# Performance work log

Hardware: AMD Instinct MI355X
Metric: run time of the kernel (lower is better)

Reference implementation:

```python
import jax, jax.numpy as jnp
import numpy as np
import math

B, N, K, S = 4, 128, 250, 250   # batch, channels(d_model), chunk len, num chunks
M = 64 // 2                      # d_state complex modes (conjugate-pair S4D param.)


def setup_inputs() -> dict:
    key = jax.random.key(0)
    ks = jax.random.split(key, 24)
    d = {"x": jax.random.normal(ks[0], (B, N, K, S), jnp.float32)}
    i = 1
    for p in ("intra", "inter"):
        # S4D (diagonal SSM) parameters
        d[p + "_log_dt"] = (jax.random.uniform(ks[i], (N,), jnp.float32)
                            * (math.log(0.1) - math.log(0.001)) + math.log(0.001))
        d[p + "_logA_re"] = jnp.full((N, M), math.log(0.5), jnp.float32)
        d[p + "_A_im"] = jnp.tile(math.pi * jnp.arange(M, dtype=jnp.float32), (N, 1))
        d[p + "_C_re"] = jax.random.normal(ks[i + 1], (N, M), jnp.float32) * (0.5 ** 0.5)
        d[p + "_C_im"] = jax.random.normal(ks[i + 2], (N, M), jnp.float32) * (0.5 ** 0.5)
        d[p + "_D"] = jax.random.normal(ks[i + 3], (N,), jnp.float32)
        # S4 output position-wise linear (H -> 2H) + GLU
        d[p + "_ow"] = jax.random.normal(ks[i + 4], (2 * N, N), jnp.float32) / math.sqrt(N)
        d[p + "_ob"] = jnp.zeros((2 * N,), jnp.float32)
        # block linear
        d[p + "_lw"] = jax.random.normal(ks[i + 5], (N, N), jnp.float32) / math.sqrt(N)
        d[p + "_lb"] = jnp.zeros((N,), jnp.float32)
        # GroupNorm(1, N)
        d[p + "_gg"] = jnp.ones((N,), jnp.float32)
        d[p + "_gb"] = jnp.zeros((N,), jnp.float32)
        i += 6
    return d


def _s4(u, log_dt, logA_re, A_im, C_re, C_im, D, ow, ob):
    # u: [b, H, L] (transposed layout). S4D kernel + FFT conv + GELU + GLU out.
    L = u.shape[-1]
    dt = jnp.exp(log_dt)                              # [H]
    A = -jnp.exp(logA_re) + 1j * A_im                 # [H, M]
    dtA = dt[:, None] * A                             # [H, M]
    C = (C_re + 1j * C_im) * (jnp.exp(dtA) - 1.0) / A # ZOH-discretized C
    vand = jnp.exp(dtA[:, :, None] * jnp.arange(L, dtype=jnp.float32))  # [H, M, L]
    kern = 2.0 * jnp.einsum('hm,hml->hl', C, vand).real                 # [H, L]
    n = 2 * L
    y = jnp.fft.irfft(jnp.fft.rfft(u, n) * jnp.fft.rfft(kern, n), n)[..., :L]
    y = y + D[:, None] * u
    y = jax.nn.gelu(y)
    y = jnp.einsum('oh,bhl->bol', ow, y) + ob[None, :, None]            # [b, 2H, L]
    y1, y2 = jnp.split(y, 2, axis=1)
    return y1 * jax.nn.sigmoid(y2)                                      # GLU -> [b, H, L]


def _group_norm(x, g, b, eps=1e-8):
    mu = jnp.mean(x, axis=(1, 2, 3), keepdims=True)
    var = jnp.var(x, axis=(1, 2, 3), keepdims=True)
    return (x - mu) / jnp.sqrt(var + eps) * g[None, :, None, None] + b[None, :, None, None]


def reference(x,
              intra_log_dt, intra_logA_re, intra_A_im, intra_C_re, intra_C_im,
              intra_D, intra_ow, intra_ob, intra_lw, intra_lb, intra_gg, intra_gb,
              inter_log_dt, inter_logA_re, inter_A_im, inter_C_re, inter_C_im,
              inter_D, inter_ow, inter_ob, inter_lw, inter_lb, inter_gg, inter_gb):
    Bx, Nx, Kx, Sx = x.shape
    # intra (within-chunk) path: sequence length = K
    intra = jnp.transpose(x, (0, 3, 1, 2)).reshape(Bx * Sx, Nx, Kx)
    intra = _s4(intra, intra_log_dt, intra_logA_re, intra_A_im,
                intra_C_re, intra_C_im, intra_D, intra_ow, intra_ob)
    # faithful to torch: .view(B*S*K, -1) on contiguous [B*S, N, K]
    intra = (intra.reshape(Bx * Sx * Kx, -1) @ intra_lw.T + intra_lb).reshape(Bx * Sx, Nx, Kx)
    intra = jnp.transpose(intra.reshape(Bx, Sx, Nx, Kx), (0, 2, 3, 1))  # [B,N,K,S]
    intra = _group_norm(intra, intra_gg, intra_gb) + x
    # inter (across-chunk) path: sequence length = S
    inter = jnp.transpose(intra, (0, 2, 1, 3)).reshape(Bx * Kx, Nx, Sx)
    inter = _s4(inter, inter_log_dt, inter_logA_re, inter_A_im,
                inter_C_re, inter_C_im, inter_D, inter_ow, inter_ob)
    inter = (inter.reshape(Bx * Kx * Sx, -1) @ inter_lw.T + inter_lb).reshape(Bx * Kx, Nx, Sx)
    inter = jnp.transpose(inter.reshape(Bx, Kx, Nx, Sx), (0, 2, 1, 3))  # [B,N,K,S]
    inter = _group_norm(inter, inter_gg, inter_gb)
    return inter + intra
```

## Files before the change

kernel.cpp:

```cpp
#include <hip/hip_runtime.h>
#include <math.h>

#define NTOT 32000000

typedef __attribute__((ext_vector_type(8))) short bf8_t;
typedef __attribute__((ext_vector_type(4))) float f4_t;

__device__ __forceinline__ float fast_tanh(float t) {
    return 1.0f - 2.0f / (1.0f + __expf(2.0f * t));
}
__device__ __forceinline__ float gelu_f(float v) {
    return 0.5f * v * (1.0f + fast_tanh(0.7978845608028654f * (v + 0.044715f * v * v * v)));
}
__device__ __forceinline__ float sigmoid_f(float v) {
    return 1.0f / (1.0f + __expf(-v));
}
__device__ __forceinline__ unsigned short f2bf(float f) {
    unsigned u = __float_as_uint(f);
    u = (u + 0x7FFFu + ((u >> 16) & 1u)) >> 16;
    return (unsigned short)u;
}
__device__ __forceinline__ float bf2f(unsigned short u) {
    return __uint_as_float(((unsigned)u) << 16);
}
__device__ __forceinline__ unsigned swz(unsigned a) {
    return a ^ (((a >> 9) & 7u) << 4);
}

__global__ void wc_kernel(const float* __restrict__ log_dt, const float* __restrict__ logA_re,
                          const float* __restrict__ A_im, const float* __restrict__ C_re,
                          const float* __restrict__ C_im, float* __restrict__ wC) {
    int t = blockIdx.x * 256 + threadIdx.x;
    if (t >= 128 * 32) return;
    int h = t >> 5, m = t & 31;
    float dt  = expf(log_dt[h]);
    float are = -expf(logA_re[t]);
    float aim = A_im[t];
    float er  = expf(dt * are);
    float wr  = er * cosf(dt * aim);
    float wi  = er * sinf(dt * aim);
    float e1r = wr - 1.0f, e1i = wi;
    float inv = 1.0f / (are * are + aim * aim);
    float qr  = (e1r * are + e1i * aim) * inv;
    float qi  = (e1i * are - e1r * aim) * inv;
    float cre = C_re[t], cim = C_im[t];
    wC[h * 128 + m]      = dt * are;
    wC[h * 128 + 32 + m] = dt * aim;
    wC[h * 128 + 64 + m] = 2.0f * (cre * qr - cim * qi);
    wC[h * 128 + 96 + m] = 2.0f * (cre * qi + cim * qr);
}

__global__ void kern_kernel(const float* __restrict__ wC, float* __restrict__ kern) {
    int h = blockIdx.x, l = threadIdx.x;
    const float* wc = wC + (h << 7);
    float acc = 0.0f;
    if (l < 250) {
        float fl = (float)l;
#pragma unroll 1
        for (int m = 0; m < 32; ++m) {
            float er  = expf(wc[m] * fl);
            float ang = wc[32 + m] * fl;
            float sv, cv;
            sincosf(ang, &sv, &cv);
            acc += er * (wc[64 + m] * cv - wc[96 + m] * sv);
        }
    }
    kern[(h << 8) + l] = acc;
}

__global__ void cvtw_kernel(const float* __restrict__ ow, const float* __restrict__ lw,
                            unsigned short* __restrict__ owbf, unsigned short* __restrict__ lwbf) {
    int t = blockIdx.x * 256 + threadIdx.x;
    if (t < 32768) owbf[t] = f2bf(ow[t]);
    else if (t < 49152) lwbf[t - 32768] = f2bf(lw[t - 32768]);
}

__global__ __launch_bounds__(256, 2)
void conv_kernel(const float* __restrict__ in, unsigned short* __restrict__ Y,
                 const float* __restrict__ kern, const float* __restrict__ Dv, int inter) {
    __shared__ unsigned short Bhi[128 * 264];
    __shared__ unsigned short Blo[128 * 40];
    __shared__ float klds[512];
    const int tid = threadIdx.x;
    const int lane = tid & 63, wave = tid >> 6;
    const int lid = lane & 15, quad = lane >> 4;
    const int s0 = blockIdx.x * 128;
    const int h = blockIdx.y, b = blockIdx.z;
    klds[tid] = 0.0f;
    klds[256 + tid] = kern[(h << 8) + tid];
    const float Dh = Dv[h];
    const float* src = in + (long)(b * 128 + h) * 62500;

    f4_t acc[4][8];
#pragma unroll
    for (int rt = 0; rt < 4; ++rt)
#pragma unroll
        for (int ct = 0; ct < 8; ++ct) acc[rt][ct] = (f4_t)0.0f;

    float2 pf[8];
    auto loadc = [&](int c) {
        if (!inter) {
#pragma unroll
            for (int it = 0; it < 8; ++it) {
                int kk = (tid >> 6) + (it << 2);
                int k = (c << 5) + kk;
                int ss = (tid & 63) << 1;
                bool v = (k < 250) && (s0 + ss < 250);
                pf[it] = v ? *(const float2*)(src + (long)k * 250 + s0 + ss)
                           : make_float2(0.0f, 0.0f);
            }
        } else {
#pragma unroll
            for (int it = 0; it < 8; ++it) {
                int kk2 = (tid >> 4) + (it << 4);
                int cc = (tid & 15) << 1;
                bool v = (s0 + kk2 < 250) && ((c << 5) + cc < 250);
                pf[it] = v ? *(const float2*)(src + (long)(s0 + kk2) * 250 + (c << 5) + cc)
                           : make_float2(0.0f, 0.0f);
            }
        }
    };
    auto storec = [&](int c) {
        if (!inter) {
#pragma unroll
            for (int it = 0; it < 8; ++it) {
                int kk = (tid >> 6) + (it << 2);
                int k = (c << 5) + kk;
                int ss = (tid & 63) << 1;
                unsigned short hx = f2bf(pf[it].x);
                unsigned short hy = f2bf(pf[it].y);
                Bhi[ss * 264 + k] = hx;
                Bhi[(ss + 1) * 264 + k] = hy;
                Blo[ss * 40 + kk] = f2bf(pf[it].x - bf2f(hx));
                Blo[(ss + 1) * 40 + kk] = f2bf(pf[it].y - bf2f(hy));
            }
        } else {
#pragma unroll
            for (int it = 0; it < 8; ++it) {
                int kk2 = (tid >> 4) + (it << 4);
                int cc = (tid & 15) << 1;
                int k = (c << 5) + cc;
                unsigned short hx = f2bf(pf[it].x);
                unsigned short hy = f2bf(pf[it].y);
                Bhi[kk2 * 264 + k] = hx;
                Bhi[kk2 * 264 + k + 1] = hy;
                Blo[kk2 * 40 + cc] = f2bf(pf[it].x - bf2f(hx));
                Blo[kk2 * 40 + cc + 1] = f2bf(pf[it].y - bf2f(hy));
            }
        }
    };

    loadc(0);
#pragma unroll 1
    for (int c = 0; c < 8; ++c) {
        __syncthreads();
        storec(c);
        __syncthreads();
        if (c < 7) loadc(c + 1);
        const int c32 = c << 5;
        bf8_t ah[4], al[4];
#pragma unroll
        for (int rt = 0; rt < 4; ++rt) {
            const int R = (rt << 6) + (wave << 4);
            if (c32 <= R + 15) {
                int d0 = 256 + R + lid - c32 - (quad << 3) - 7;
                float r[8];
#pragma unroll
                for (int j = 0; j < 8; ++j) r[j] = klds[d0 + j];
#pragma unroll
                for (int j = 0; j < 8; ++j) {
                    float v = r[7 - j];
                    unsigned short hb = f2bf(v);
                    ah[rt][j] = (short)hb;
                    al[rt][j] = (short)f2bf(v - bf2f(hb));
                }
            }
        }
#pragma unroll
        for (int ct = 0; ct < 8; ++ct) {
            bf8_t bh = *(const bf8_t*)(Bhi + (ct * 16 + lid) * 264 + c32 + (quad << 3));
            bf8_t bl = *(const bf8_t*)(Blo + (ct * 16 + lid) * 40 + (quad << 3));
#pragma unroll
            for (int rt = 0; rt < 4; ++rt) {
                const int R = (rt << 6) + (wave << 4);
                if (c32 <= R + 15) {
                    acc[rt][ct] = __builtin_amdgcn_mfma_f32_16x16x32_bf16(ah[rt], bh, acc[rt][ct], 0, 0, 0);
                    acc[rt][ct] = __builtin_amdgcn_mfma_f32_16x16x32_bf16(ah[rt], bl, acc[rt][ct], 0, 0, 0);
                    acc[rt][ct] = __builtin_amdgcn_mfma_f32_16x16x32_bf16(al[rt], bh, acc[rt][ct], 0, 0, 0);
                }
            }
        }
    }
    __syncthreads();
#pragma unroll
    for (int rt = 0; rt < 4; ++rt) {
        const int Rq = (rt << 6) + (wave << 4) + (quad << 2);
#pragma unroll
        for (int ct = 0; ct < 8; ++ct) {
            const int sl = ct * 16 + lid;
#pragma unroll
            for (int reg = 0; reg < 4; ++reg) {
                int row = Rq + reg;
                float u = bf2f(Bhi[sl * 264 + row]);
                float y = acc[rt][ct][reg] + Dh * u;
                Bhi[sl * 264 + row] = f2bf(gelu_f(y));
            }
        }
    }
    __syncthreads();
    const unsigned int* Bu = (const unsigned int*)Bhi;
    unsigned int* Yg = (unsigned int*)Y + ((long)(b * 250 + s0) * 128 + h) * 125;
#pragma unroll 1
    for (int i = tid; i < 16384; i += 256) {
        int sl = i >> 7, e = i & 127;
        if (e < 125 && s0 + sl < 250)
            Yg[(long)sl * 16000 + e] = Bu[sl * 132 + e];
    }
}

__global__ __launch_bounds__(256, 2)
void mlp_kernel(const unsigned short* __restrict__ Ybf, const unsigned short* __restrict__ owbf,
                const float* __restrict__ ob, const unsigned short* __restrict__ lwbf,
                const float* __restrict__ lb, float* __restrict__ V, double* __restrict__ part) {
    __shared__ unsigned short ZL[32768];
    __shared__ unsigned short Yt[32 * 136];
    const int tid = threadIdx.x;
    const int lane = tid & 63, wave = tid >> 6;
    const int lid = lane & 15, quad = lane >> 4;
    const int seq = blockIdx.x;
    const unsigned short* Ys = Ybf + (long)seq * 32000;

    const int tb0 = 2 * wave;
    int tmap[4] = {tb0, tb0 + 1, tb0 + 8, tb0 + 9};
    bf8_t wf[4][4];
#pragma unroll
    for (int c = 0; c < 4; ++c)
#pragma unroll
        for (int t = 0; t < 4; ++t)
            wf[c][t] = *(const bf8_t*)(owbf + (tmap[t] * 16 + lid) * 128 + c * 32 + quad * 8);
    float ob1[2][4], ob2[2][4];
#pragma unroll
    for (int p = 0; p < 2; ++p)
#pragma unroll
        for (int reg = 0; reg < 4; ++reg) {
            int o = tmap[p] * 16 + quad * 4 + reg;
            ob1[p][reg] = ob[o];
            ob2[p][reg] = ob[128 + o];
        }

    unsigned int pf[8];
    auto loadc = [&](int l0) {
#pragma unroll
        for (int it = 0; it < 8; ++it) {
            int i = tid + it * 256;
            int h = i >> 4;
            int l = l0 + (i & 15) * 2;
            pf[it] = (l < 250) ? *(const unsigned int*)(Ys + h * 250 + l) : 0u;
        }
    };
    auto storec = [&]() {
#pragma unroll
        for (int it = 0; it < 8; ++it) {
            int i = tid + it * 256;
            int h = i >> 4;
            int l2 = (i & 15) * 2;
            Yt[l2 * 136 + h] = (unsigned short)(pf[it] & 0xFFFF);
            Yt[(l2 + 1) * 136 + h] = (unsigned short)(pf[it] >> 16);
        }
    };

    loadc(0);
#pragma unroll 1
    for (int ch = 0; ch < 8; ++ch) {
        __syncthreads();
        storec();
        __syncthreads();
        if (ch < 7) loadc((ch + 1) * 32);
        f4_t acc[4][2];
#pragma unroll
        for (int t = 0; t < 4; ++t)
#pragma unroll
            for (int jj = 0; jj < 2; ++jj) acc[t][jj] = (f4_t)0.0f;
#pragma unroll
        for (int c = 0; c < 4; ++c) {
            bf8_t bfr[2];
#pragma unroll
            for (int jj = 0; jj < 2; ++jj)
                bfr[jj] = *(const bf8_t*)(Yt + (jj * 16 + lid) * 136 + c * 32 + quad * 8);
#pragma unroll
            for (int t = 0; t < 4; ++t)
#pragma unroll
                for (int jj = 0; jj < 2; ++jj)
                    acc[t][jj] = __builtin_amdgcn_mfma_f32_16x16x32_bf16(wf[c][t], bfr[jj], acc[t][jj], 0, 0, 0);
        }
        const int lbase = ch * 32;
#pragma unroll
        for (int p = 0; p < 2; ++p) {
            int ob0 = tmap[p] * 16 + quad * 4;
#pragma unroll
            for (int reg = 0; reg < 4; ++reg) {
                int o = ob0 + reg;
#pragma unroll
                for (int jj = 0; jj < 2; ++jj) {
                    int l = lbase + jj * 16 + lid;
                    if (l < 250) {
                        float z1 = acc[p][jj][reg] + ob1[p][reg];
                        float z2 = acc[p + 2][jj][reg] + ob2[p][reg];
                        unsigned a = swz((unsigned)(o * 250 + l) * 2u);
                        *(unsigned short*)((char*)ZL + a) = f2bf(z1 * sigmoid_f(z2));
                    }
                }
            }
        }
    }
    __syncthreads();

    f4_t acc2[4][8];
#pragma unroll
    for (int mt = 0; mt < 4; ++mt)
#pragma unroll
        for (int nt = 0; nt < 8; ++nt) acc2[mt][nt] = (f4_t)0.0f;
    const int j0 = wave * 64;
#pragma unroll
    for (int c = 0; c < 4; ++c) {
        bf8_t af[4];
#pragma unroll
        for (int mt = 0; mt < 4; ++mt) {
            unsigned a = swz((unsigned)((j0 + mt * 16 + lid) * 128 + c * 32 + quad * 8) * 2u);
            af[mt] = *(const bf8_t*)((char*)ZL + a);
        }
#pragma unroll
        for (int nt = 0; nt < 8; ++nt) {
            bf8_t bfr = *(const bf8_t*)(lwbf + (nt * 16 + lid) * 128 + c * 32 + quad * 8);
#pragma unroll
            for (int mt = 0; mt < 4; ++mt)
                acc2[mt][nt] = __builtin_amdgcn_mfma_f32_16x16x32_bf16(af[mt], bfr, acc2[mt][nt], 0, 0, 0);
        }
    }
    double s = 0.0, q = 0.0;
    float* Vs = V + (long)seq * 32000;
#pragma unroll
    for (int nt = 0; nt < 8; ++nt) {
        int o = nt * 16 + lid;
        float bb = lb[o];
#pragma unroll
        for (int mt = 0; mt < 4; ++mt)
#pragma unroll
            for (int reg = 0; reg < 4; ++reg) {
                int j = j0 + mt * 16 + quad * 4 + reg;
                if (j < 250) {
                    float v = acc2[mt][nt][reg] + bb;
                    Vs[j * 128 + o] = v;
                    s += (double)v;
                    q += (double)v * (double)v;
                }
            }
    }
    __syncthreads();
    double* red = (double*)Yt;
    red[tid] = s;
    red[256 + tid] = q;
    __syncthreads();
    for (int st = 128; st > 0; st >>= 1) {
        if (tid < st) {
            red[tid] += red[tid + st];
            red[256 + tid] += red[256 + tid + st];
        }
        __syncthreads();
    }
    if (tid == 0) {
        part[seq * 2] = red[0];
        part[seq * 2 + 1] = red[256];
    }
}

__global__ void stats_final_kernel(const double* __restrict__ part, float* __restrict__ stats) {
    __shared__ double ssum[256], ssq[256];
    const int b = blockIdx.x;
    double s = 0.0, q = 0.0;
    if (threadIdx.x < 250) {
        s = part[(b * 250 + threadIdx.x) * 2];
        q = part[(b * 250 + threadIdx.x) * 2 + 1];
    }
    ssum[threadIdx.x] = s; ssq[threadIdx.x] = q;
    __syncthreads();
    for (int st = 128; st > 0; st >>= 1) {
        if (threadIdx.x < st) {
            ssum[threadIdx.x] += ssum[threadIdx.x + st];
            ssq[threadIdx.x]  += ssq[threadIdx.x + st];
        }
        __syncthreads();
    }
    if (threadIdx.x == 0) {
        double mu = ssum[0] / 8000000.0;
        double var = ssq[0] / 8000000.0 - mu * mu;
        stats[b * 2] = (float)mu;
        stats[b * 2 + 1] = (float)(1.0 / sqrt(var + 1e-8));
    }
}

__global__ void intra_fin_kernel(const float* __restrict__ f, const float* __restrict__ x,
                                 const float* __restrict__ stats, const float* __restrict__ gg,
                                 const float* __restrict__ gb, float* __restrict__ out) {
    __shared__ float tile[32][33];
    int kt = blockIdx.x, st = blockIdx.y;
    int bn = blockIdx.z; int b = bn >> 7, n = bn & 127;
    int tx = threadIdx.x & 31, ty = threadIdx.x >> 5;
    const float mu = stats[b * 2], rs = stats[b * 2 + 1];
    const float ga = gg[n] * rs, bb = gb[n];
    const float* fb = f + (long)(b * 250) * 32000 + n * 250;
#pragma unroll
    for (int j = 0; j < 4; ++j) {
        int k = kt * 32 + tx;
        int s = st * 32 + ty + j * 8;
        if (k < 250 && s < 250) tile[ty + j * 8][tx] = fb[(long)s * 32000 + k];
    }
    __syncthreads();
#pragma unroll
    for (int j = 0; j < 4; ++j) {
        int s = st * 32 + tx;
        int k = kt * 32 + ty + j * 8;
        if (k < 250 && s < 250) {
            long idx = ((long)(b * 128 + n) * 250 + k) * 250 + s;
            out[idx] = (tile[tx][ty + j * 8] - mu) * ga + bb + x[idx];
        }
    }
}

__global__ void final_kernel(const float* __restrict__ f2, const float* __restrict__ stats,
                             const float* __restrict__ gg, const float* __restrict__ gb,
                             float* __restrict__ out) {
    long g = (long)blockIdx.x * 256 + threadIdx.x;
    if (g >= NTOT) return;
    int s = (int)(g % 250); long r = g / 250;
    int k = (int)(r % 250); long bn = r / 250;
    int n = (int)(bn % 128); int b = (int)(bn / 128);
    float mu = stats[b * 2], rs = stats[b * 2 + 1];
    float v = f2[((long)(b * 250 + k) * 128 + n) * 250 + s];
    out[g] = (v - mu) * rs * gg[n] + gb[n] + out[g];
}

extern "C" void kernel_launch(void* const* d_in, const int* in_sizes, int n_in,
                              void* d_out, int out_size, void* d_ws, size_t ws_size,
                              hipStream_t stream) {
    (void)in_sizes; (void)n_in; (void)out_size; (void)ws_size;
    const float* x = (const float*)d_in[0];
    float* out = (float*)d_out;
    char* base = (char*)d_ws;
    float* V            = (float*)base;
    unsigned short* Ybf = (unsigned short*)(base + 128000000L);
    float* wC           = (float*)(base + 256000000L);
    unsigned short* owbf= (unsigned short*)(base + 256065536L);
    unsigned short* lwbf= (unsigned short*)(base + 256131072L);
    double* part        = (double*)(base + 256163840L);
    float* stats        = (float*)(base + 256180224L);
    float* kern         = (float*)(base + 120000000L);

    const float* i_logdt = (const float*)d_in[1];
    const float* i_logA  = (const float*)d_in[2];
    const float* i_Aim   = (const float*)d_in[3];
    const float* i_Cre   = (const float*)d_in[4];
    const float* i_Cim   = (const float*)d_in[5];
    const float* i_D     = (const float*)d_in[6];
    const float* i_ow    = (const float*)d_in[7];
    const float* i_ob    = (const float*)d_in[8];
    const float* i_lw    = (const float*)d_in[9];
    const float* i_lb    = (const float*)d_in[10];
    const float* i_gg    = (const float*)d_in[11];
    const float* i_gb    = (const float*)d_in[12];
    const float* e_logdt = (const float*)d_in[13];
    const float* e_logA  = (const float*)d_in[14];
    const float* e_Aim   = (const float*)d_in[15];
    const float* e_Cre   = (const float*)d_in[16];
    const float* e_Cim   = (const float*)d_in[17];
    const float* e_D     = (const float*)d_in[18];
    const float* e_ow    = (const float*)d_in[19];
    const float* e_ob    = (const float*)d_in[20];
    const float* e_lw    = (const float*)d_in[21];
    const float* e_lb    = (const float*)d_in[22];
    const float* e_gg    = (const float*)d_in[23];
    const float* e_gb    = (const float*)d_in[24];

    wc_kernel<<<16, 256, 0, stream>>>(i_logdt, i_logA, i_Aim, i_Cre, i_Cim, wC);
    kern_kernel<<<128, 256, 0, stream>>>(wC, kern);
    cvtw_kernel<<<192, 256, 0, stream>>>(i_ow, i_lw, owbf, lwbf);
    conv_kernel<<<dim3(2, 128, 4), 256, 0, stream>>>(x, Ybf, kern, i_D, 0);
    mlp_kernel<<<1000, 256, 0, stream>>>(Ybf, owbf, i_ob, lwbf, i_lb, V, part);
    stats_final_kernel<<<4, 256, 0, stream>>>(part, stats);
    intra_fin_kernel<<<dim3(8, 8, 512), 256, 0, stream>>>(V, x, stats, i_gg, i_gb, out);

    wc_kernel<<<16, 256, 0, stream>>>(e_logdt, e_logA, e_Aim, e_Cre, e_Cim, wC);
    kern_kernel<<<128, 256, 0, stream>>>(wC, kern);
    cvtw_kernel<<<192, 256, 0, stream>>>(e_ow, e_lw, owbf, lwbf);
    conv_kernel<<<dim3(2, 128, 4), 256, 0, stream>>>(out, Ybf, kern, e_D, 1);
    mlp_kernel<<<1000, 256, 0, stream>>>(Ybf, owbf, e_ob, lwbf, e_lb, V, part);
    stats_final_kernel<<<4, 256, 0, stream>>>(part, stats);
    final_kernel<<<NTOT / 256, 256, 0, stream>>>(V, stats, e_gg, e_gb, out);
}
```

Baseline: 811.4 us.

## Precompute Toeplitz kernel fragments and retile causal conv with swizzled LDS

Folds the D skip term into kernel tap zero and adds a frag_kernel that precomputes hi/lo bf16 MFMA A-fragments of the Toeplitz convolution matrix in global memory. The conv kernel then loads those fragments directly instead of rebuilding them per block from LDS. The conv tile shrinks to 64 sequences per block with a new wave-to-tile mapping, doubling the grid and allowing 3 blocks per CU. The input tile moves to an XOR-swizzled unpadded LDS layout with packed stores, and the epilogue no longer re-reads u for the D term. The cost is an extra small launch and global fragment reads, which are likely to hit in L2.

```diff
diff --git a/kernel.cpp b/kernel.cpp
--- a/kernel.cpp
+++ b/kernel.cpp
@@ -50,7 +50,8 @@
     wC[h * 128 + 96 + m] = 2.0f * (cre * qi + cim * qr);
 }
 
-__global__ void kern_kernel(const float* __restrict__ wC, float* __restrict__ kern) {
+__global__ void kern_kernel(const float* __restrict__ wC, const float* __restrict__ Dv,
+                            float* __restrict__ kern) {
     int h = blockIdx.x, l = threadIdx.x;
     const float* wc = wC + (h << 7);
     float acc = 0.0f;
@@ -64,8 +65,28 @@
             sincosf(ang, &sv, &cv);
             acc += er * (wc[64 + m] * cv - wc[96 + m] * sv);
         }
+        if (l == 0) acc += Dv[h];
     }
     kern[(h << 8) + l] = acc;
+}
+
+__global__ void frag_kernel(const float* __restrict__ kern, unsigned short* __restrict__ fragH,
+                            unsigned short* __restrict__ fragL) {
+    int h = blockIdx.x, d16 = blockIdx.y, lane = threadIdx.x;
+    int lid = lane & 15, q = lane >> 4;
+    const float* kh = kern + (h << 8);
+    bf8_t vh, vl;
+#pragma unroll
+    for (int j = 0; j < 8; ++j) {
+        int idx = d16 * 16 + lid - 8 * q - j;
+        float v = (idx >= 0) ? kh[idx] : 0.0f;
+        unsigned short hb = f2bf(v);
+        vh[j] = (short)hb;
+        vl[j] = (short)f2bf(v - bf2f(hb));
+    }
+    long off = ((long)((h << 4) + d16) * 64 + lane) * 8;
+    *(bf8_t*)(fragH + off) = vh;
+    *(bf8_t*)(fragL + off) = vl;
 }
 
 __global__ void cvtw_kernel(const float* __restrict__ ow, const float* __restrict__ lw,
@@ -75,47 +96,50 @@
     else if (t < 49152) lwbf[t - 32768] = f2bf(lw[t - 32768]);
 }
 
-__global__ __launch_bounds__(256, 2)
+__global__ __launch_bounds__(256, 3)
 void conv_kernel(const float* __restrict__ in, unsigned short* __restrict__ Y,
-                 const float* __restrict__ kern, const float* __restrict__ Dv, int inter) {
-    __shared__ unsigned short Bhi[128 * 264];
-    __shared__ unsigned short Blo[128 * 40];
-    __shared__ float klds[512];
+                 const unsigned short* __restrict__ fragH, const unsigned short* __restrict__ fragL,
+                 int inter) {
+    __shared__ unsigned short Bhi[64 * 256];
+    __shared__ unsigned short Blo[64 * 40];
     const int tid = threadIdx.x;
     const int lane = tid & 63, wave = tid >> 6;
     const int lid = lane & 15, quad = lane >> 4;
-    const int s0 = blockIdx.x * 128;
+    const int a = wave >> 1, p = wave & 1;
+    const int s0 = blockIdx.x * 64;
     const int h = blockIdx.y, b = blockIdx.z;
-    klds[tid] = 0.0f;
-    klds[256 + tid] = kern[(h << 8) + tid];
-    const float Dh = Dv[h];
     const float* src = in + (long)(b * 128 + h) * 62500;
-
-    f4_t acc[4][8];
+    char* BhiB = (char*)Bhi;
+    char* BloB = (char*)Blo;
+
+    f4_t acc[4][4];
 #pragma unroll
     for (int rt = 0; rt < 4; ++rt)
 #pragma unroll
-        for (int ct = 0; ct < 8; ++ct) acc[rt][ct] = (f4_t)0.0f;
-
-    float2 pf[8];
+        for (int ct = 0; ct < 4; ++ct) acc[rt][ct] = (f4_t)0.0f;
+
+    float2 pf[4];
     auto loadc = [&](int c) {
         if (!inter) {
 #pragma unroll
-            for (int it = 0; it < 8; ++it) {
-                int kk = (tid >> 6) + (it << 2);
+            for (int it = 0; it < 4; ++it) {
+                int i = tid + it * 256;
+                int kk = i >> 5;
+                int sp = (i & 31) << 1;
                 int k = (c << 5) + kk;
-                int ss = (tid & 63) << 1;
-                bool v = (k < 250) && (s0 + ss < 250);
-                pf[it] = v ? *(const float2*)(src + (long)k * 250 + s0 + ss)
+                bool v = (k < 250) && (s0 + sp < 250);
+                pf[it] = v ? *(const float2*)(src + (long)k * 250 + s0 + sp)
                            : make_float2(0.0f, 0.0f);
             }
         } else {
 #pragma unroll
-            for (int it = 0; it < 8; ++it) {
-                int kk2 = (tid >> 4) + (it << 4);
-                int cc = (tid & 15) << 1;
-                bool v = (s0 + kk2 < 250) && ((c << 5) + cc < 250);
-                pf[it] = v ? *(const float2*)(src + (long)(s0 + kk2) * 250 + (c << 5) + cc)
+            for (int it = 0; it < 4; ++it) {
+                int i = tid + it * 256;
+                int sq = i >> 4;
+                int tt = (i & 15) << 1;
+                int t = (c << 5) + tt;
+                bool v = (s0 + sq < 250) && (t < 250);
+                pf[it] = v ? *(const float2*)(src + (long)(s0 + sq) * 250 + t)
                            : make_float2(0.0f, 0.0f);
             }
         }
@@ -123,29 +147,34 @@
     auto storec = [&](int c) {
         if (!inter) {
 #pragma unroll
-            for (int it = 0; it < 8; ++it) {
-                int kk = (tid >> 6) + (it << 2);
+            for (int it = 0; it < 4; ++it) {
+                int i = tid + it * 256;
+                int kk = i >> 5;
+                int sp = (i & 31) << 1;
                 int k = (c << 5) + kk;
-                int ss = (tid & 63) << 1;
                 unsigned short hx = f2bf(pf[it].x);
                 unsigned short hy = f2bf(pf[it].y);
-                Bhi[ss * 264 + k] = hx;
-                Bhi[(ss + 1) * 264 + k] = hy;
-                Blo[ss * 40 + kk] = f2bf(pf[it].x - bf2f(hx));
-                Blo[(ss + 1) * 40 + kk] = f2bf(pf[it].y - bf2f(hy));
+                unsigned b0 = (unsigned)(sp * 512 + k * 2) ^ ((unsigned)(sp & 7) << 4);
+                unsigned b1 = (unsigned)((sp + 1) * 512 + k * 2) ^ ((unsigned)((sp + 1) & 7) << 4);
+                *(unsigned short*)(BhiB + b0) = hx;
+                *(unsigned short*)(BhiB + b1) = hy;
+                Blo[sp * 40 + kk] = f2bf(pf[it].x - bf2f(hx));
+                Blo[(sp + 1) * 40 + kk] = f2bf(pf[it].y - bf2f(hy));
             }
         } else {
 #pragma unroll
-            for (int it = 0; it < 8; ++it) {
-                int kk2 = (tid >> 4) + (it << 4);
-                int cc = (tid & 15) << 1;
-                int k = (c << 5) + cc;
+            for (int it = 0; it < 4; ++it) {
+                int i = tid + it * 256;
+                int sq = i >> 4;
+                int tt = (i & 15) << 1;
                 unsigned short hx = f2bf(pf[it].x);
                 unsigned short hy = f2bf(pf[it].y);
-                Bhi[kk2 * 264 + k] = hx;
-                Bhi[kk2 * 264 + k + 1] = hy;
-                Blo[kk2 * 40 + cc] = f2bf(pf[it].x - bf2f(hx));
-                Blo[kk2 * 40 + cc + 1] = f2bf(pf[it].y - bf2f(hy));
+                unsigned hpack = (unsigned)hx | ((unsigned)hy << 16);
+                unsigned b0 = (unsigned)(sq * 512 + ((c << 5) + tt) * 2) ^ ((unsigned)(sq & 7) << 4);
+                *(unsigned*)(BhiB + b0) = hpack;
+                unsigned short lx = f2bf(pf[it].x - bf2f(hx));
+                unsigned short ly = f2bf(pf[it].y - bf2f(hy));
+                *(unsigned*)(BloB + sq * 80 + tt * 2) = (unsigned)lx | ((unsigned)ly << 16);
             }
         }
     };
@@ -157,64 +186,54 @@
         storec(c);
         __syncthreads();
         if (c < 7) loadc(c + 1);
-        const int c32 = c << 5;
-        bf8_t ah[4], al[4];
+        bf8_t bh[4], bl[4];
+#pragma unroll
+        for (int ct = 0; ct < 4; ++ct) {
+            int row = ct * 16 + lid;
+            unsigned byteB = (unsigned)(row * 512 + c * 64 + quad * 16) ^ ((unsigned)(row & 7) << 4);
+            bh[ct] = *(const bf8_t*)(BhiB + byteB);
+            bl[ct] = *(const bf8_t*)(BloB + row * 80 + quad * 16);
+        }
 #pragma unroll
         for (int rt = 0; rt < 4; ++rt) {
-            const int R = (rt << 6) + (wave << 4);
-            if (c32 <= R + 15) {
-                int d0 = 256 + R + lid - c32 - (quad << 3) - 7;
-                float r[8];
-#pragma unroll
-                for (int j = 0; j < 8; ++j) r[j] = klds[d0 + j];
-#pragma unroll
-                for (int j = 0; j < 8; ++j) {
-                    float v = r[7 - j];
-                    unsigned short hb = f2bf(v);
-                    ah[rt][j] = (short)hb;
-                    al[rt][j] = (short)f2bf(v - bf2f(hb));
+            int n = 2 * rt + a - c;
+            if (n >= 0) {
+                long fo = ((long)((h << 4) + 2 * n + p) * 64 + lane) * 8;
+                bf8_t fh = *(const bf8_t*)(fragH + fo);
+                bf8_t fl = *(const bf8_t*)(fragL + fo);
+#pragma unroll
+                for (int ct = 0; ct < 4; ++ct) {
+                    acc[rt][ct] = __builtin_amdgcn_mfma_f32_16x16x32_bf16(fh, bh[ct], acc[rt][ct], 0, 0, 0);
+                    acc[rt][ct] = __builtin_amdgcn_mfma_f32_16x16x32_bf16(fh, bl[ct], acc[rt][ct], 0, 0, 0);
+                    acc[rt][ct] = __builtin_amdgcn_mfma_f32_16x16x32_bf16(fl, bh[ct], acc[rt][ct], 0, 0, 0);
                 }
             }
         }
-#pragma unroll
-        for (int ct = 0; ct < 8; ++ct) {
-            bf8_t bh = *(const bf8_t*)(Bhi + (ct * 16 + lid) * 264 + c32 + (quad << 3));
-            bf8_t bl = *(const bf8_t*)(Blo + (ct * 16 + lid) * 40 + (quad << 3));
-#pragma unroll
-            for (int rt = 0; rt < 4; ++rt) {
-                const int R = (rt << 6) + (wave << 4);
-                if (c32 <= R + 15) {
-                    acc[rt][ct] = __builtin_amdgcn_mfma_f32_16x16x32_bf16(ah[rt], bh, acc[rt][ct], 0, 0, 0);
-                    acc[rt][ct] = __builtin_amdgcn_mfma_f32_16x16x32_bf16(ah[rt], bl, acc[rt][ct], 0, 0, 0);
-                    acc[rt][ct] = __builtin_amdgcn_mfma_f32_16x16x32_bf16(al[rt], bh, acc[rt][ct], 0, 0, 0);
-                }
-            }
-        }
     }
     __syncthreads();
 #pragma unroll
     for (int rt = 0; rt < 4; ++rt) {
-        const int Rq = (rt << 6) + (wave << 4) + (quad << 2);
-#pragma unroll
-        for (int ct = 0; ct < 8; ++ct) {
-            const int sl = ct * 16 + lid;
-#pragma unroll
-            for (int reg = 0; reg < 4; ++reg) {
-                int row = Rq + reg;
-                float u = bf2f(Bhi[sl * 264 + row]);
-                float y = acc[rt][ct][reg] + Dh * u;
-                Bhi[sl * 264 + row] = f2bf(gelu_f(y));
-            }
-        }
-    }
-    __syncthreads();
-    const unsigned int* Bu = (const unsigned int*)Bhi;
+        const int l0 = rt * 64 + wave * 16 + quad * 4;
+#pragma unroll
+        for (int ct = 0; ct < 4; ++ct) {
+            const int sq = ct * 16 + lid;
+            unsigned lo = (unsigned)f2bf(gelu_f(acc[rt][ct][0])) |
+                          ((unsigned)f2bf(gelu_f(acc[rt][ct][1])) << 16);
+            unsigned hi = (unsigned)f2bf(gelu_f(acc[rt][ct][2])) |
+                          ((unsigned)f2bf(gelu_f(acc[rt][ct][3])) << 16);
+            unsigned byteO = (unsigned)(sq * 512 + l0 * 2) ^ ((unsigned)(sq & 7) << 4);
+            *(uint2*)(BhiB + byteO) = make_uint2(lo, hi);
+        }
+    }
+    __syncthreads();
     unsigned int* Yg = (unsigned int*)Y + ((long)(b * 250 + s0) * 128 + h) * 125;
 #pragma unroll 1
-    for (int i = tid; i < 16384; i += 256) {
-        int sl = i >> 7, e = i & 127;
-        if (e < 125 && s0 + sl < 250)
-            Yg[(long)sl * 16000 + e] = Bu[sl * 132 + e];
+    for (int i = tid; i < 8192; i += 256) {
+        int sq = i >> 7, e = i & 127;
+        if (e < 125 && s0 + sq < 250) {
+            unsigned v = *(unsigned*)(BhiB + ((unsigned)(sq * 512 + e * 4) ^ ((unsigned)(sq & 7) << 4)));
+            Yg[(long)sq * 16000 + e] = v;
+        }
     }
 }
 
@@ -240,12 +259,12 @@
             wf[c][t] = *(const bf8_t*)(owbf + (tmap[t] * 16 + lid) * 128 + c * 32 + quad * 8);
     float ob1[2][4], ob2[2][4];
 #pragma unroll
-    for (int p = 0; p < 2; ++p)
+    for (int pp = 0; pp < 2; ++pp)
 #pragma unroll
         for (int reg = 0; reg < 4; ++reg) {
-            int o = tmap[p] * 16 + quad * 4 + reg;
-            ob1[p][reg] = ob[o];
-            ob2[p][reg] = ob[128 + o];
+            int o = tmap[pp] * 16 + quad * 4 + reg;
+            ob1[pp][reg] = ob[o];
+            ob2[pp][reg] = ob[128 + o];
         }
 
     unsigned int pf[8];
@@ -253,19 +272,19 @@
 #pragma unroll
         for (int it = 0; it < 8; ++it) {
             int i = tid + it * 256;
-            int h = i >> 4;
+            int hh = i >> 4;
             int l = l0 + (i & 15) * 2;
-            pf[it] = (l < 250) ? *(const unsigned int*)(Ys + h * 250 + l) : 0u;
+            pf[it] = (l < 250) ? *(const unsigned int*)(Ys + hh * 250 + l) : 0u;
         }
     };
     auto storec = [&]() {
 #pragma unroll
         for (int it = 0; it < 8; ++it) {
             int i = tid + it * 256;
-            int h = i >> 4;
+            int hh = i >> 4;
             int l2 = (i & 15) * 2;
-            Yt[l2 * 136 + h] = (unsigned short)(pf[it] & 0xFFFF);
-            Yt[(l2 + 1) * 136 + h] = (unsigned short)(pf[it] >> 16);
+            Yt[l2 * 136 + hh] = (unsigned short)(pf[it] & 0xFFFF);
+            Yt[(l2 + 1) * 136 + hh] = (unsigned short)(pf[it] >> 16);
         }
     };
 
@@ -295,19 +314,18 @@
         }
         const int lbase = ch * 32;
 #pragma unroll
-        for (int p = 0; p < 2; ++p) {
-            int ob0 = tmap[p] * 16 + quad * 4;
+        for (int pp = 0; pp < 2; ++pp) {
 #pragma unroll
             for (int reg = 0; reg < 4; ++reg) {
-                int o = ob0 + reg;
+                int o = tmap[pp] * 16 + quad * 4 + reg;
 #pragma unroll
                 for (int jj = 0; jj < 2; ++jj) {
                     int l = lbase + jj * 16 + lid;
                     if (l < 250) {
-                        float z1 = acc[p][jj][reg] + ob1[p][reg];
-                        float z2 = acc[p + 2][jj][reg] + ob2[p][reg];
-                        unsigned a = swz((unsigned)(o * 250 + l) * 2u);
-                        *(unsigned short*)((char*)ZL + a) = f2bf(z1 * sigmoid_f(z2));
+                        float z1 = acc[pp][jj][reg] + ob1[pp][reg];
+                        float z2 = acc[pp + 2][jj][reg] + ob2[pp][reg];
+                        unsigned aB = swz((unsigned)(o * 250 + l) * 2u);
+                        *(unsigned short*)((char*)ZL + aB) = f2bf(z1 * sigmoid_f(z2));
                     }
                 }
             }
@@ -326,8 +344,8 @@
         bf8_t af[4];
 #pragma unroll
         for (int mt = 0; mt < 4; ++mt) {
-            unsigned a = swz((unsigned)((j0 + mt * 16 + lid) * 128 + c * 32 + quad * 8) * 2u);
-            af[mt] = *(const bf8_t*)((char*)ZL + a);
+            unsigned aB = swz((unsigned)((j0 + mt * 16 + lid) * 128 + c * 32 + quad * 8) * 2u);
+            af[mt] = *(const bf8_t*)((char*)ZL + aB);
         }
 #pragma unroll
         for (int nt = 0; nt < 8; ++nt) {
@@ -454,7 +472,9 @@
     unsigned short* lwbf= (unsigned short*)(base + 256131072L);
     double* part        = (double*)(base + 256163840L);
     float* stats        = (float*)(base + 256180224L);
-    float* kern         = (float*)(base + 120000000L);
+    float* kern         = (float*)(base + 118000000L);
+    unsigned short* fragH = (unsigned short*)(base + 120000000L);
+    unsigned short* fragL = (unsigned short*)(base + 123000000L);
 
     const float* i_logdt = (const float*)d_in[1];
     const float* i_logA  = (const float*)d_in[2];
@@ -482,17 +502,19 @@
     const float* e_gb    = (const float*)d_in[24];
 
     wc_kernel<<<16, 256, 0, stream>>>(i_logdt, i_logA, i_Aim, i_Cre, i_Cim, wC);
-    kern_kernel<<<128, 256, 0, stream>>>(wC, kern);
+    kern_kernel<<<128, 256, 0, stream>>>(wC, i_D, kern);
+    frag_kernel<<<dim3(128, 16), 64, 0, stream>>>(kern, fragH, fragL);
     cvtw_kernel<<<192, 256, 0, stream>>>(i_ow, i_lw, owbf, lwbf);
-    conv_kernel<<<dim3(2, 128, 4), 256, 0, stream>>>(x, Ybf, kern, i_D, 0);
+    conv_kernel<<<dim3(4, 128, 4), 256, 0, stream>>>(x, Ybf, fragH, fragL, 0);
     mlp_kernel<<<1000, 256, 0, stream>>>(Ybf, owbf, i_ob, lwbf, i_lb, V, part);
     stats_final_kernel<<<4, 256, 0, stream>>>(part, stats);
     intra_fin_kernel<<<dim3(8, 8, 512), 256, 0, stream>>>(V, x, stats, i_gg, i_gb, out);
 
     wc_kernel<<<16, 256, 0, stream>>>(e_logdt, e_logA, e_Aim, e_Cre, e_Cim, wC);
-    kern_kernel<<<128, 256, 0, stream>>>(wC, kern);
+    kern_kernel<<<128, 256, 0, stream>>>(wC, e_D, kern);
+    frag_kernel<<<dim3(128, 16), 64, 0, stream>>>(kern, fragH, fragL);
     cvtw_kernel<<<192, 256, 0, stream>>>(e_ow, e_lw, owbf, lwbf);
-    conv_kernel<<<dim3(2, 128, 4), 256, 0, stream>>>(out, Ybf, kern, e_D, 1);
+    conv_kernel<<<dim3(4, 128, 4), 256, 0, stream>>>(out, Ybf, fragH, fragL, 1);
     mlp_kernel<<<1000, 256, 0, stream>>>(Ybf, owbf, e_ob, lwbf, e_lb, V, part);
     stats_final_kernel<<<4, 256, 0, stream>>>(part, stats);
     final_kernel<<<NTOT / 256, 256, 0, stream>>>(V, stats, e_gg, e_gb, out);
```

Measured after the change: 841.1 us. 1.04x slower.
